# Performance work log

Hardware: AMD Instinct MI355X
Metric: run time of the kernel (lower is better)

## Reference

```python
import jax, jax.numpy as jnp
import numpy as np

B, T, C = 128, 256, 384
H, D = 6, 64

def setup_inputs() -> dict:
    key = jax.random.key(0)
    ks = jax.random.split(key, 6)
    s = 1.0 / np.sqrt(C)
    return {
        "x": jax.random.normal(ks[0], (B, T, C), dtype=jnp.float32),
        "Wq": jax.random.normal(ks[1], (H, C, D), dtype=jnp.float32) * s,
        "Wk": jax.random.normal(ks[2], (H, C, D), dtype=jnp.float32) * s,
        "Wv": jax.random.normal(ks[3], (H, C, D), dtype=jnp.float32) * s,
        "Wp": jax.random.normal(ks[4], (C, C), dtype=jnp.float32) * s,
        "bp": jnp.zeros((C,), dtype=jnp.float32),
    }

def reference(x, Wq, Wk, Wv, Wp, bp):
    # per-head projections (all heads at once): [B,T,C] x [H,C,D] -> [B,H,T,D]
    q = jnp.einsum("btc,hcd->bhtd", x, Wq)
    k = jnp.einsum("btc,hcd->bhtd", x, Wk)
    v = jnp.einsum("btc,hcd->bhtd", x, Wv)
    scale = 1.0 / jnp.sqrt(jnp.asarray(D, dtype=x.dtype))
    # scores [B,H,T,T], causal mask, softmax
    wei = jnp.einsum("bhqd,bhkd->bhqk", q, k) * scale
    causal = jnp.tril(jnp.ones((T, T), dtype=bool))
    wei = jnp.where(causal, wei, -jnp.inf)
    wei = jax.nn.softmax(wei, axis=-1)
    # dropout layers are identity in eval mode
    out = jnp.einsum("bhqk,bhkd->bhqd", wei, v)
    # concat heads: [B,T,H*D]
    out = out.transpose(0, 2, 1, 3).reshape(B, T, H * D)
    return out @ Wp + bp
```

## Files before the change

### kernel.cpp

```cpp
#include <hip/hip_runtime.h>
#include <stdint.h>


typedef __attribute__((ext_vector_type(8))) short bf16x8;
typedef __attribute__((ext_vector_type(4))) float f32x4;
typedef __attribute__((ext_vector_type(16))) float f32x16;

__device__ __forceinline__ unsigned short f2b(float f) {
    union { float f; unsigned int u; } v; v.f = f;
    unsigned int u = v.u + 0x7fffu + ((v.u >> 16) & 1u);
    return (unsigned short)(u >> 16);
}

__device__ __forceinline__ unsigned int pk2(float lo, float hi) {
    return (unsigned int)f2b(lo) | ((unsigned int)f2b(hi) << 16);
}

__device__ __forceinline__ uint32_t cvtpk(float lo, float hi) {
    uint32_t r;
    asm("v_cvt_pk_bf16_f32 %0, %1, %2" : "=v"(r) : "v"(lo), "v"(hi));
    return r;
}

__device__ __forceinline__ void gload_lds16(const void* g, void* lds) {
    auto gp = reinterpret_cast<const __attribute__((address_space(1))) uint32_t*>(
        reinterpret_cast<uintptr_t>(g));
    auto lp = reinterpret_cast<__attribute__((address_space(3))) uint32_t*>(
        reinterpret_cast<uintptr_t>(lds));
    __builtin_amdgcn_global_load_lds(gp, lp, 16, 0, 0);
}

#define SBAR0() __builtin_amdgcn_sched_barrier(0)


__global__ void cvt_w_kernel(const float* __restrict__ Wq, const float* __restrict__ Wk,
                             const float* __restrict__ Wv, const float* __restrict__ Wp,
                             unsigned short* __restrict__ wt, unsigned short* __restrict__ wpt) {
    int i = blockIdx.x * 256 + threadIdx.x;
    if (i >= 589824) return;
    if (i < 442368) {
        int j = i / 384, c = i - j * 384;
        int p = j / 384, rem = j - p * 384;
        int h = rem >> 6, d = rem & 63;
        const float* W = (p == 0) ? Wq : ((p == 1) ? Wk : Wv);
        wt[i] = f2b(W[(size_t)(h * 384 + c) * 64 + d]);
    } else {
        int i2 = i - 442368;
        int n = i2 / 384, c = i2 - n * 384;
        wpt[i2] = f2b(Wp[(size_t)c * 384 + n]);
    }
}


__global__ __launch_bounds__(256, 4) void gemm_qkv(
    const float* __restrict__ x,
    const unsigned short* __restrict__ wt,
    unsigned short* __restrict__ qO,
    unsigned short* __restrict__ kO,
    unsigned short* __restrict__ vO)
{
    extern __shared__ __align__(16) unsigned short smem[];
    unsigned short* As0 = smem;
    unsigned short* As1 = smem + 4096;
    unsigned short* Bs0 = smem + 8192;
    unsigned short* Bs1 = smem + 12288;

    const int tid  = threadIdx.x;
    const int lane = tid & 63;
    const int w    = tid >> 6;
    const int wm = w >> 1, wn = w & 1;

    const int flat = blockIdx.y * 9 + blockIdx.x;
    const int swz = (flat & 7) * 288 + (flat >> 3);
    const int bx = swz % 9, by = swz / 9;
    const int col0 = bx * 128;
    const int row0 = by * 128;

    f32x4 acc[4][4];
#pragma unroll
    for (int mf = 0; mf < 4; ++mf)
#pragma unroll
        for (int nf = 0; nf < 4; ++nf)
#pragma unroll
            for (int r = 0; r < 4; ++r) acc[mf][nf][r] = 0.f;

    const int ci0 = tid;
    const int ci1 = tid + 256;
    const float* aS0 = x + (size_t)(row0 + (ci0 >> 2)) * 384 + (ci0 & 3) * 8;
    const float* aS1 = x + (size_t)(row0 + (ci1 >> 2)) * 384 + (ci1 & 3) * 8;
    const unsigned short* bS0 = wt + (size_t)(col0 + (ci0 >> 2)) * 384 + (ci0 & 3) * 8;
    const unsigned short* bS1 = wt + (size_t)(col0 + (ci1 >> 2)) * 384 + (ci1 & 3) * 8;
    const int cb = w * 64;

    float4 aReg0, aReg1, aReg2, aReg3;
    auto LOADA = [&](int kt) {
        const float* p0 = aS0 + kt * 32;
        const float* p1 = aS1 + kt * 32;
        aReg0 = *(const float4*)(p0);
        aReg1 = *(const float4*)(p0 + 4);
        aReg2 = *(const float4*)(p1);
        aReg3 = *(const float4*)(p1 + 4);
    };
    auto WRITEA = [&](unsigned short* As) {
        uint4 w0, w1;
        w0.x = cvtpk(aReg0.x, aReg0.y); w0.y = cvtpk(aReg0.z, aReg0.w);
        w0.z = cvtpk(aReg1.x, aReg1.y); w0.w = cvtpk(aReg1.z, aReg1.w);
        w1.x = cvtpk(aReg2.x, aReg2.y); w1.y = cvtpk(aReg2.z, aReg2.w);
        w1.z = cvtpk(aReg3.x, aReg3.y); w1.w = cvtpk(aReg3.z, aReg3.w);
        *(uint4*)&As[ci0 * 8] = w0;
        *(uint4*)&As[ci1 * 8] = w1;
    };
    auto STAGEB = [&](unsigned short* Bs, int kt) {
        gload_lds16(bS0 + kt * 32, Bs + (cb + 0) * 8);
        gload_lds16(bS1 + kt * 32, Bs + (cb + 256) * 8);
    };
    auto COMPUTE = [&](const unsigned short* A, const unsigned short* B) {
        bf16x8 aF[4], bF[4];
#pragma unroll
        for (int mf = 0; mf < 4; ++mf)
            aF[mf] = *(const bf16x8*)&A[(wm * 64 + mf * 16 + (lane & 15)) * 32 + (lane >> 4) * 8];
#pragma unroll
        for (int nf = 0; nf < 4; ++nf)
            bF[nf] = *(const bf16x8*)&B[(wn * 64 + nf * 16 + (lane & 15)) * 32 + (lane >> 4) * 8];
#pragma unroll
        for (int mf = 0; mf < 4; ++mf)
#pragma unroll
            for (int nf = 0; nf < 4; ++nf)
                acc[mf][nf] = __builtin_amdgcn_mfma_f32_16x16x32_bf16(aF[mf], bF[nf], acc[mf][nf], 0, 0, 0);
    };

    LOADA(0);
    STAGEB(Bs0, 0);
    WRITEA(As0);
    __syncthreads();

    for (int t = 0; t < 12; ++t) {
        unsigned short* Acur = (t & 1) ? As1 : As0;
        unsigned short* Bcur = (t & 1) ? Bs1 : Bs0;
        unsigned short* Anx  = (t & 1) ? As0 : As1;
        unsigned short* Bnx  = (t & 1) ? Bs0 : Bs1;
        if (t < 11) {
            LOADA(t + 1);
            STAGEB(Bnx, t + 1);
        }
        COMPUTE(Acur, Bcur);
        if (t < 11) WRITEA(Anx);
        __syncthreads();
    }

    unsigned short* Ct = smem;
    const int co = tid & 15;
    const int rr = tid >> 4;
    const int colg = col0 + co * 8;
    const int p = colg / 384;
    const int rem = colg - p * 384;
    const int h = rem >> 6;
    const int d = rem & 63;
    unsigned short* dst = (p == 0) ? qO : ((p == 1) ? kO : vO);

#pragma unroll
    for (int ph = 0; ph < 2; ++ph) {
        if (wm == ph) {
#pragma unroll
            for (int mf = 0; mf < 4; ++mf)
#pragma unroll
                for (int nf = 0; nf < 4; ++nf)
#pragma unroll
                    for (int r = 0; r < 4; ++r)
                        Ct[(mf * 16 + (lane >> 4) * 4 + r) * 136 + wn * 64 + nf * 16 + (lane & 15)] =
                            f2b(acc[mf][nf][r]);
        }
        __syncthreads();
#pragma unroll
        for (int it = 0; it < 4; ++it) {
            const int r_loc = it * 16 + rr;
            const int m = row0 + ph * 64 + r_loc;
            const int b = m >> 8, t = m & 255;
            uint4 val = *(const uint4*)&Ct[r_loc * 136 + co * 8];
            *(uint4*)&dst[(size_t)((b * 6 + h) * 256 + t) * 64 + d] = val;
        }
        __syncthreads();
    }
}


__global__ __launch_bounds__(512, 4) void attn_kernel(
    const unsigned short* __restrict__ Qg,
    const unsigned short* __restrict__ Kg,
    const unsigned short* __restrict__ Vg,
    unsigned short* __restrict__ Og)
{
    extern __shared__ __align__(16) unsigned short asmem[];
    unsigned short* Ks = asmem;
    unsigned short* Vs = asmem + 256 * 72;
    unsigned short* Ot = asmem;
    const int bh = blockIdx.x;
    const int b = bh / 6, h = bh - b * 6;
    const int tid = threadIdx.x;
    const int lane = tid & 63;
    const int w = tid >> 6;
    const int lo = lane & 31, hi = lane >> 5;

    const unsigned short* kg = Kg + (size_t)bh * 256 * 64;
#pragma unroll
    for (int j = 0; j < 4; ++j) {
        int chunk = tid + 512 * j;
        int key = chunk >> 3, dc = (chunk & 7) * 8;
        *(uint4*)&Ks[key * 72 + dc] = *(const uint4*)&kg[key * 64 + dc];
    }
    {
        const unsigned short* vg = Vg + (size_t)bh * 256 * 64;
        uint32_t* Vs32 = (uint32_t*)Vs;
#pragma unroll
        for (int i = 0; i < 2; ++i) {
            int u = tid + 512 * i;
            int t2 = (u & 31) | ((u >> 8) << 5);
            int dm = (u >> 5) & 7;
            uint4 r0 = *(const uint4*)&vg[(2 * t2 + 0) * 64 + dm * 8];
            uint4 r1 = *(const uint4*)&vg[(2 * t2 + 1) * 64 + dm * 8];
            const unsigned short* e0 = (const unsigned short*)&r0;
            const unsigned short* e1 = (const unsigned short*)&r1;
#pragma unroll
            for (int j = 0; j < 8; ++j)
                Vs32[(dm * 8 + j) * 132 + t2] = (uint32_t)e0[j] | ((uint32_t)e1[j] << 16);
        }
    }
    __syncthreads();

    const int q0 = w * 32;
    const unsigned short* qg = Qg + (size_t)bh * 256 * 64 + (size_t)(q0 + lo) * 64 + hi * 8;
    bf16x8 qF[4];
#pragma unroll
    for (int dc = 0; dc < 4; ++dc) qF[dc] = *(const bf16x8*)(qg + dc * 16);

    float m = -1e30f, ssum = 0.f;
    f32x16 o0, o1;
#pragma unroll
    for (int r = 0; r < 16; ++r) { o0[r] = 0.f; o1[r] = 0.f; }

    for (int kt = 0; kt <= w; ++kt) {
        f32x16 s;
#pragma unroll
        for (int r = 0; r < 16; ++r) s[r] = 0.f;
        __builtin_amdgcn_s_setprio(1);
#pragma unroll
        for (int dc = 0; dc < 4; ++dc) {
            bf16x8 aK = *(const bf16x8*)&Ks[(kt * 32 + lo) * 72 + dc * 16 + hi * 8];
            s = __builtin_amdgcn_mfma_f32_32x32x16_bf16(aK, qF[dc], s, 0, 0, 0);
        }
        __builtin_amdgcn_s_setprio(0);
        float p[16];
        float pmax = -1e30f;
        const bool diag = (kt == w);
#pragma unroll
        for (int r = 0; r < 16; ++r) {
            float sv = s[r] * 0.125f;
            const int keyl = (r & 3) + 8 * (r >> 2) + 4 * hi;
            if (diag && keyl > lo) sv = -1e30f;
            p[r] = sv;
            pmax = fmaxf(pmax, sv);
        }
        pmax = fmaxf(pmax, __shfl_xor(pmax, 32, 64));
        if (pmax > m + 8.f) {
            const float sf = __expf(m - pmax);
            m = pmax;
            ssum *= sf;
#pragma unroll
            for (int r = 0; r < 16; ++r) { o0[r] *= sf; o1[r] *= sf; }
        }
        float rs = 0.f;
#pragma unroll
        for (int r = 0; r < 16; ++r) { p[r] = __expf(p[r] - m); rs += p[r]; }
        rs += __shfl_xor(rs, 32, 64);
        ssum += rs;

        union { unsigned short u[16]; bf16x8 v[2]; } P;
        {
            float recv[4];
#pragma unroll
            for (int j2 = 0; j2 < 4; ++j2) {
                float sendv = hi ? p[j2] : p[4 + j2];
                recv[j2] = __shfl_xor(sendv, 32, 64);
            }
#pragma unroll
            for (int i = 0; i < 4; ++i) P.u[i]     = f2b(hi ? recv[i] : p[i]);
#pragma unroll
            for (int i = 0; i < 4; ++i) P.u[4 + i] = f2b(hi ? p[4 + i] : recv[i]);
        }
        {
            float recv[4];
#pragma unroll
            for (int j2 = 0; j2 < 4; ++j2) {
                float sendv = hi ? p[8 + j2] : p[12 + j2];
                recv[j2] = __shfl_xor(sendv, 32, 64);
            }
#pragma unroll
            for (int i = 0; i < 4; ++i) P.u[8 + i]  = f2b(hi ? recv[i] : p[8 + i]);
#pragma unroll
            for (int i = 0; i < 4; ++i) P.u[12 + i] = f2b(hi ? p[12 + i] : recv[i]);
        }

        __builtin_amdgcn_s_setprio(1);
#pragma unroll
        for (int kc = 0; kc < 2; ++kc) {
            bf16x8 aV0 = *(const bf16x8*)&Vs[lo * 264 + kt * 32 + kc * 16 + hi * 8];
            o0 = __builtin_amdgcn_mfma_f32_32x32x16_bf16(aV0, P.v[kc], o0, 0, 0, 0);
            bf16x8 aV1 = *(const bf16x8*)&Vs[(32 + lo) * 264 + kt * 32 + kc * 16 + hi * 8];
            o1 = __builtin_amdgcn_mfma_f32_32x32x16_bf16(aV1, P.v[kc], o1, 0, 0, 0);
        }
        __builtin_amdgcn_s_setprio(0);
    }

    __syncthreads();
    const float inv = 1.f / ssum;
    {
        uint32_t* ot32 = (uint32_t*)&Ot[w * 32 * 72];
#pragma unroll
        for (int g = 0; g < 4; ++g) {
            const int dbase0 = 8 * g + 4 * hi;
            uint32_t w0 = pk2(o0[4 * g + 0] * inv, o0[4 * g + 1] * inv);
            uint32_t w1 = pk2(o0[4 * g + 2] * inv, o0[4 * g + 3] * inv);
            int dw = lo * 36 + (dbase0 >> 1);
            ot32[dw] = w0;
            ot32[dw + 1] = w1;
            uint32_t w2 = pk2(o1[4 * g + 0] * inv, o1[4 * g + 1] * inv);
            uint32_t w3 = pk2(o1[4 * g + 2] * inv, o1[4 * g + 3] * inv);
            int dw1 = lo * 36 + ((32 + dbase0) >> 1);
            ot32[dw1] = w2;
            ot32[dw1 + 1] = w3;
        }
    }
    __syncthreads();
    {
        const unsigned short* ot = &Ot[w * 32 * 72];
        const int q = lane >> 1;
        const int half = (lane & 1) * 32;
        unsigned short* og = Og + (size_t)(b * 256 + q0 + q) * 384 + h * 64 + half;
#pragma unroll
        for (int jj = 0; jj < 4; ++jj) {
            uint4 val = *(const uint4*)&ot[q * 72 + half + jj * 8];
            *(uint4*)&og[jj * 8] = val;
        }
    }
}


__global__ __launch_bounds__(256, 3) void gemm_proj(
    const unsigned short* __restrict__ ob,
    const unsigned short* __restrict__ wpt,
    const float* __restrict__ bp,
    float* __restrict__ out)
{
    __shared__ __align__(16) unsigned short As[3][128 * 32];
    __shared__ __align__(16) unsigned short Bs[3][128 * 32];
    const int tid  = threadIdx.x;
    const int lane = tid & 63;
    const int w    = tid >> 6;
    const int wm = w >> 1, wn = w & 1;

    const int flat = blockIdx.y * 3 + blockIdx.x;
    const int swz = (flat & 7) * 96 + (flat >> 3);
    const int bx = swz % 3, by = swz / 3;
    const int col0 = bx * 128;
    const int row0 = by * 128;

    const unsigned short* Abase = ob  + (size_t)row0 * 384;
    const unsigned short* Bbase = wpt + (size_t)col0 * 384;

    f32x4 acc[4][4];
#pragma unroll
    for (int mf = 0; mf < 4; ++mf)
#pragma unroll
        for (int nf = 0; nf < 4; ++nf)
#pragma unroll
            for (int r = 0; r < 4; ++r) acc[mf][nf][r] = 0.f;

    const int ci0 = tid;
    const int ci1 = tid + 256;
    const int r0c = ci0 >> 2, o0c = (ci0 & 3) ^ ((ci0 >> 3) & 3);
    const int r1c = ci1 >> 2, o1c = (ci1 & 3) ^ ((ci1 >> 3) & 3);
    const unsigned short* aSrc0 = Abase + (size_t)r0c * 384 + o0c * 8;
    const unsigned short* aSrc1 = Abase + (size_t)r1c * 384 + o1c * 8;
    const unsigned short* bSrc0 = Bbase + (size_t)r0c * 384 + o0c * 8;
    const unsigned short* bSrc1 = Bbase + (size_t)r1c * 384 + o1c * 8;
    const int cb = w * 64;

    auto STAGE = [&](int buf, int kt) {
        const int k0_ = kt * 32;
        gload_lds16(aSrc0 + k0_, (unsigned short*)As[buf] + (cb + 0) * 8);
        gload_lds16(bSrc0 + k0_, (unsigned short*)Bs[buf] + (cb + 0) * 8);
        gload_lds16(aSrc1 + k0_, (unsigned short*)As[buf] + (cb + 256) * 8);
        gload_lds16(bSrc1 + k0_, (unsigned short*)Bs[buf] + (cb + 256) * 8);
    };

    const int fr = lane & 15;
    const int oc = (lane >> 4) ^ ((fr >> 1) & 3);

    auto COMPUTE = [&](int buf) {
        const unsigned short* A = As[buf];
        const unsigned short* B = Bs[buf];
        bf16x8 aF[4], bF[4];
#pragma unroll
        for (int mf = 0; mf < 4; ++mf)
            aF[mf] = *(const bf16x8*)&A[(wm * 64 + mf * 16 + fr) * 32 + oc * 8];
#pragma unroll
        for (int nf = 0; nf < 4; ++nf)
            bF[nf] = *(const bf16x8*)&B[(wn * 64 + nf * 16 + fr) * 32 + oc * 8];
#pragma unroll
        for (int mf = 0; mf < 4; ++mf)
#pragma unroll
            for (int nf = 0; nf < 4; ++nf)
                acc[mf][nf] = __builtin_amdgcn_mfma_f32_16x16x32_bf16(aF[mf], bF[nf], acc[mf][nf], 0, 0, 0);
    };

    STAGE(0, 0);
    STAGE(1, 1);
    SBAR0();
    int bufS = 2, bufC = 0;
    for (int t = 0; t < 10; ++t) {
        STAGE(bufS, t + 2);
        bufS = (bufS == 2) ? 0 : bufS + 1;
        SBAR0();
        asm volatile("s_waitcnt vmcnt(8)" ::: "memory");
        SBAR0();
        __builtin_amdgcn_s_barrier();
        SBAR0();
        COMPUTE(bufC);
        bufC = (bufC == 2) ? 0 : bufC + 1;
        SBAR0();
        __builtin_amdgcn_s_barrier();
        SBAR0();
    }
    asm volatile("s_waitcnt vmcnt(4)" ::: "memory");
    SBAR0();
    __builtin_amdgcn_s_barrier();
    SBAR0();
    COMPUTE(1);
    SBAR0();
    __builtin_amdgcn_s_barrier();
    SBAR0();
    asm volatile("s_waitcnt vmcnt(0)" ::: "memory");
    SBAR0();
    __builtin_amdgcn_s_barrier();
    SBAR0();
    COMPUTE(2);

#pragma unroll
    for (int nf = 0; nf < 4; ++nf) {
        const int col = col0 + wn * 64 + nf * 16 + (lane & 15);
        const float bias = bp[col];
#pragma unroll
        for (int mf = 0; mf < 4; ++mf) {
            const int mbase = row0 + wm * 64 + mf * 16 + ((lane >> 4) * 4);
#pragma unroll
            for (int r = 0; r < 4; ++r) {
                const int mrow = mbase + r;
                out[(size_t)mrow * 384 + col] = acc[mf][nf][r] + bias;
            }
        }
    }
}


extern "C" void kernel_launch(void* const* d_in, const int* in_sizes, int n_in,
                              void* d_out, int out_size, void* d_ws, size_t ws_size,
                              hipStream_t stream) {
    const float* x  = (const float*)d_in[0];
    const float* Wq = (const float*)d_in[1];
    const float* Wk = (const float*)d_in[2];
    const float* Wv = (const float*)d_in[3];
    const float* Wp = (const float*)d_in[4];
    const float* bp = (const float*)d_in[5];
    float* out = (float*)d_out;

    char* ws = (char*)d_ws;
    unsigned short* ob  = (unsigned short*)(ws);
    unsigned short* qb  = (unsigned short*)(ws + 25165824);
    unsigned short* kb  = (unsigned short*)(ws + 50331648);
    unsigned short* vb  = (unsigned short*)(ws + 75497472);
    unsigned short* wt  = (unsigned short*)(ws + 100663296);
    unsigned short* wpt = (unsigned short*)(ws + 101548032);

    cvt_w_kernel<<<2304, 256, 0, stream>>>(Wq, Wk, Wv, Wp, wt, wpt);
    gemm_qkv<<<dim3(9, 256), 256, 32768, stream>>>(x, wt, qb, kb, vb);
    attn_kernel<<<768, 512, 70656, stream>>>(qb, kb, vb, ob);
    gemm_proj<<<dim3(3, 256), 256, 0, stream>>>(ob, wpt, bp, out);
}
```

Before: 105.2 us.

## Fuse QKV projection into attention kernel per batch-head block

Each attention block now computes its own head's Q, K and V projections from x via MFMA and writes them straight into LDS, eliminating the separate QKV GEMM kernel and its global Q/K/V writes and reads. It also swizzles the LDS staging layout to reduce bank conflicts. In exchange x is re-read once per head, the block uses about 128 KB of LDS limiting occupancy to one block per CU, and the GEMM tile per block is small and serialized before attention.

```diff
diff --git a/kernel.cpp b/kernel.cpp
--- a/kernel.cpp
+++ b/kernel.cpp
@@ -52,45 +52,58 @@
 }
 
 
-__global__ __launch_bounds__(256, 4) void gemm_qkv(
+__global__ __launch_bounds__(512, 1) void qkv_attn(
     const float* __restrict__ x,
-    const unsigned short* __restrict__ wt,
-    unsigned short* __restrict__ qO,
-    unsigned short* __restrict__ kO,
-    unsigned short* __restrict__ vO)
+    const unsigned short* __restrict__ wtb,
+    unsigned short* __restrict__ Og)
 {
-    extern __shared__ __align__(16) unsigned short smem[];
-    unsigned short* As0 = smem;
-    unsigned short* As1 = smem + 4096;
-    unsigned short* Bs0 = smem + 8192;
-    unsigned short* Bs1 = smem + 12288;
-
-    const int tid  = threadIdx.x;
+    extern __shared__ __align__(16) unsigned short fsm[];
+    unsigned short* Ks  = fsm;
+    unsigned short* Vs  = fsm + 18432;
+    unsigned short* Stg = fsm + 35328;
+    unsigned short* As0 = Stg;
+    unsigned short* As1 = Stg + 8192;
+    unsigned short* Bs0 = Stg + 16384;
+    unsigned short* Bs1 = Stg + 22528;
+    unsigned short* Qs  = Stg;
+    unsigned short* Ot  = Stg;
+
+    const int bh = blockIdx.x;
+    const int b = bh / 6, h = bh - b * 6;
+    const int tid = threadIdx.x;
     const int lane = tid & 63;
-    const int w    = tid >> 6;
+    const int w = tid >> 6;
     const int wm = w >> 1, wn = w & 1;
-
-    const int flat = blockIdx.y * 9 + blockIdx.x;
-    const int swz = (flat & 7) * 288 + (flat >> 3);
-    const int bx = swz % 9, by = swz / 9;
-    const int col0 = bx * 128;
-    const int row0 = by * 128;
-
-    f32x4 acc[4][4];
+    const int fr = lane & 15, q4 = lane >> 4;
+    const int lo = lane & 31, hi = lane >> 5;
+
+    const float* xrow = x + (size_t)b * 256 * 384;
+
+    const int aci0 = tid, aci1 = tid + 512;
+    const int ar0 = aci0 >> 2, aog0 = aci0 & 3;
+    const int ar1 = aci1 >> 2, aog1 = aci1 & 3;
+    const float* aS0 = xrow + (size_t)ar0 * 384 + aog0 * 8;
+    const float* aS1 = xrow + (size_t)ar1 * 384 + aog1 * 8;
+    const int ad0 = ar0 * 32 + (aog0 ^ ((ar0 >> 1) & 3)) * 8;
+    const int ad1 = ar1 * 32 + (aog1 ^ ((ar1 >> 1) & 3)) * 8;
+
+    const int bci0 = tid;
+    const int bp0 = bci0 >> 8, brs0 = (bci0 >> 2) & 63;
+    const int bog0 = (bci0 & 3) ^ ((bci0 >> 3) & 3);
+    const unsigned short* bS0 = wtb + (size_t)(bp0 * 384 + h * 64 + brs0) * 384 + bog0 * 8;
+    const int bci1 = 512 + tid;
+    const int bp1 = bci1 >> 8, brs1 = (bci1 >> 2) & 63;
+    const int bog1 = (bci1 & 3) ^ ((bci1 >> 3) & 3);
+    const unsigned short* bS1 = wtb + (size_t)(bp1 * 384 + h * 64 + brs1) * 384 + bog1 * 8;
+    const int cbB = w * 64;
+
+    f32x4 acc[4][6];
 #pragma unroll
     for (int mf = 0; mf < 4; ++mf)
 #pragma unroll
-        for (int nf = 0; nf < 4; ++nf)
+        for (int nf = 0; nf < 6; ++nf)
 #pragma unroll
             for (int r = 0; r < 4; ++r) acc[mf][nf][r] = 0.f;
-
-    const int ci0 = tid;
-    const int ci1 = tid + 256;
-    const float* aS0 = x + (size_t)(row0 + (ci0 >> 2)) * 384 + (ci0 & 3) * 8;
-    const float* aS1 = x + (size_t)(row0 + (ci1 >> 2)) * 384 + (ci1 & 3) * 8;
-    const unsigned short* bS0 = wt + (size_t)(col0 + (ci0 >> 2)) * 384 + (ci0 & 3) * 8;
-    const unsigned short* bS1 = wt + (size_t)(col0 + (ci1 >> 2)) * 384 + (ci1 & 3) * 8;
-    const int cb = w * 64;
 
     float4 aReg0, aReg1, aReg2, aReg3;
     auto LOADA = [&](int kt) {
@@ -107,25 +120,26 @@
         w0.z = cvtpk(aReg1.x, aReg1.y); w0.w = cvtpk(aReg1.z, aReg1.w);
         w1.x = cvtpk(aReg2.x, aReg2.y); w1.y = cvtpk(aReg2.z, aReg2.w);
         w1.z = cvtpk(aReg3.x, aReg3.y); w1.w = cvtpk(aReg3.z, aReg3.w);
-        *(uint4*)&As[ci0 * 8] = w0;
-        *(uint4*)&As[ci1 * 8] = w1;
+        *(uint4*)&As[ad0] = w0;
+        *(uint4*)&As[ad1] = w1;
     };
     auto STAGEB = [&](unsigned short* Bs, int kt) {
-        gload_lds16(bS0 + kt * 32, Bs + (cb + 0) * 8);
-        gload_lds16(bS1 + kt * 32, Bs + (cb + 256) * 8);
-    };
+        gload_lds16(bS0 + kt * 32, Bs + cbB * 8);
+        if (tid < 256) gload_lds16(bS1 + kt * 32, Bs + (512 + cbB) * 8);
+    };
+    const int ocf = q4 ^ ((fr >> 1) & 3);
     auto COMPUTE = [&](const unsigned short* A, const unsigned short* B) {
-        bf16x8 aF[4], bF[4];
+        bf16x8 aF[4], bF[6];
 #pragma unroll
         for (int mf = 0; mf < 4; ++mf)
-            aF[mf] = *(const bf16x8*)&A[(wm * 64 + mf * 16 + (lane & 15)) * 32 + (lane >> 4) * 8];
-#pragma unroll
-        for (int nf = 0; nf < 4; ++nf)
-            bF[nf] = *(const bf16x8*)&B[(wn * 64 + nf * 16 + (lane & 15)) * 32 + (lane >> 4) * 8];
+            aF[mf] = *(const bf16x8*)&A[(wm * 64 + mf * 16 + fr) * 32 + ocf * 8];
+#pragma unroll
+        for (int nf = 0; nf < 6; ++nf)
+            bF[nf] = *(const bf16x8*)&B[(wn * 96 + nf * 16 + fr) * 32 + ocf * 8];
 #pragma unroll
         for (int mf = 0; mf < 4; ++mf)
 #pragma unroll
-            for (int nf = 0; nf < 4; ++nf)
+            for (int nf = 0; nf < 6; ++nf)
                 acc[mf][nf] = __builtin_amdgcn_mfma_f32_16x16x32_bf16(aF[mf], bF[nf], acc[mf][nf], 0, 0, 0);
     };
 
@@ -148,90 +162,31 @@
         __syncthreads();
     }
 
-    unsigned short* Ct = smem;
-    const int co = tid & 15;
-    const int rr = tid >> 4;
-    const int colg = col0 + co * 8;
-    const int p = colg / 384;
-    const int rem = colg - p * 384;
-    const int h = rem >> 6;
-    const int d = rem & 63;
-    unsigned short* dst = (p == 0) ? qO : ((p == 1) ? kO : vO);
-
-#pragma unroll
-    for (int ph = 0; ph < 2; ++ph) {
-        if (wm == ph) {
-#pragma unroll
-            for (int mf = 0; mf < 4; ++mf)
-#pragma unroll
-                for (int nf = 0; nf < 4; ++nf)
-#pragma unroll
-                    for (int r = 0; r < 4; ++r)
-                        Ct[(mf * 16 + (lane >> 4) * 4 + r) * 136 + wn * 64 + nf * 16 + (lane & 15)] =
-                            f2b(acc[mf][nf][r]);
-        }
-        __syncthreads();
-#pragma unroll
-        for (int it = 0; it < 4; ++it) {
-            const int r_loc = it * 16 + rr;
-            const int m = row0 + ph * 64 + r_loc;
-            const int b = m >> 8, t = m & 255;
-            uint4 val = *(const uint4*)&Ct[r_loc * 136 + co * 8];
-            *(uint4*)&dst[(size_t)((b * 6 + h) * 256 + t) * 64 + d] = val;
-        }
-        __syncthreads();
-    }
-}
-
-
-__global__ __launch_bounds__(512, 4) void attn_kernel(
-    const unsigned short* __restrict__ Qg,
-    const unsigned short* __restrict__ Kg,
-    const unsigned short* __restrict__ Vg,
-    unsigned short* __restrict__ Og)
-{
-    extern __shared__ __align__(16) unsigned short asmem[];
-    unsigned short* Ks = asmem;
-    unsigned short* Vs = asmem + 256 * 72;
-    unsigned short* Ot = asmem;
-    const int bh = blockIdx.x;
-    const int b = bh / 6, h = bh - b * 6;
-    const int tid = threadIdx.x;
-    const int lane = tid & 63;
-    const int w = tid >> 6;
-    const int lo = lane & 31, hi = lane >> 5;
-
-    const unsigned short* kg = Kg + (size_t)bh * 256 * 64;
-#pragma unroll
-    for (int j = 0; j < 4; ++j) {
-        int chunk = tid + 512 * j;
-        int key = chunk >> 3, dc = (chunk & 7) * 8;
-        *(uint4*)&Ks[key * 72 + dc] = *(const uint4*)&kg[key * 64 + dc];
-    }
-    {
-        const unsigned short* vg = Vg + (size_t)bh * 256 * 64;
-        uint32_t* Vs32 = (uint32_t*)Vs;
-#pragma unroll
-        for (int i = 0; i < 2; ++i) {
-            int u = tid + 512 * i;
-            int t2 = (u & 31) | ((u >> 8) << 5);
-            int dm = (u >> 5) & 7;
-            uint4 r0 = *(const uint4*)&vg[(2 * t2 + 0) * 64 + dm * 8];
-            uint4 r1 = *(const uint4*)&vg[(2 * t2 + 1) * 64 + dm * 8];
-            const unsigned short* e0 = (const unsigned short*)&r0;
-            const unsigned short* e1 = (const unsigned short*)&r1;
-#pragma unroll
-            for (int j = 0; j < 8; ++j)
-                Vs32[(dm * 8 + j) * 132 + t2] = (uint32_t)e0[j] | ((uint32_t)e1[j] << 16);
+#pragma unroll
+    for (int nf = 0; nf < 6; ++nf) {
+        const int jbase = wn * 96 + nf * 16;
+        const int tgt = jbase >> 6;
+        const int d = (jbase & 63) + fr;
+#pragma unroll
+        for (int mf = 0; mf < 4; ++mf) {
+            const int tb = wm * 64 + mf * 16 + q4 * 4;
+#pragma unroll
+            for (int r = 0; r < 4; ++r) {
+                const unsigned short val = f2b(acc[mf][nf][r]);
+                const int t = tb + r;
+                if (tgt == 0)      Qs[t * 72 + d] = val;
+                else if (tgt == 1) Ks[t * 72 + d] = val;
+                else               Vs[d * 264 + t] = val;
+            }
         }
     }
     __syncthreads();
 
     const int q0 = w * 32;
-    const unsigned short* qg = Qg + (size_t)bh * 256 * 64 + (size_t)(q0 + lo) * 64 + hi * 8;
     bf16x8 qF[4];
 #pragma unroll
-    for (int dc = 0; dc < 4; ++dc) qF[dc] = *(const bf16x8*)(qg + dc * 16);
+    for (int dc = 0; dc < 4; ++dc)
+        qF[dc] = *(const bf16x8*)&Qs[(q0 + lo) * 72 + dc * 16 + hi * 8];
 
     float m = -1e30f, ssum = 0.f;
     f32x16 o0, o1;
@@ -475,14 +430,10 @@
 
     char* ws = (char*)d_ws;
     unsigned short* ob  = (unsigned short*)(ws);
-    unsigned short* qb  = (unsigned short*)(ws + 25165824);
-    unsigned short* kb  = (unsigned short*)(ws + 50331648);
-    unsigned short* vb  = (unsigned short*)(ws + 75497472);
-    unsigned short* wt  = (unsigned short*)(ws + 100663296);
-    unsigned short* wpt = (unsigned short*)(ws + 101548032);
+    unsigned short* wt  = (unsigned short*)(ws + 25165824);
+    unsigned short* wpt = (unsigned short*)(ws + 26050560);
 
     cvt_w_kernel<<<2304, 256, 0, stream>>>(Wq, Wk, Wv, Wp, wt, wpt);
-    gemm_qkv<<<dim3(9, 256), 256, 32768, stream>>>(x, wt, qb, kb, vb);
-    attn_kernel<<<768, 512, 70656, stream>>>(qb, kb, vb, ob);
+    qkv_attn<<<768, 512, 128000, stream>>>(x, wt, ob);
     gemm_proj<<<dim3(3, 256), 256, 0, stream>>>(ob, wpt, bp, out);
 }
```

Result: slower. 119.6 us (+13.7%).

## Double K-tile depth in QKV GEMM and XOR-swizzle LDS layout

Applied to the files above, without the earlier changes.

The QKV projection GEMM now stages a 64-wide K slice per iteration instead of 32, which halves the number of main-loop iterations and barriers. The LDS tiles for A and B use an XOR swizzle on 16-byte chunks to avoid bank conflicts when the MFMA fragments are read. Shared memory per block doubles to 64KB and launch bounds drop from 4 to 2 blocks per CU, so occupancy falls in exchange for fewer syncs and conflict-free LDS reads.

```diff
diff --git a/kernel.cpp b/kernel.cpp
--- a/kernel.cpp
+++ b/kernel.cpp
@@ -52,7 +52,7 @@
 }
 
 
-__global__ __launch_bounds__(256, 4) void gemm_qkv(
+__global__ __launch_bounds__(256, 2) void gemm_qkv(
     const float* __restrict__ x,
     const unsigned short* __restrict__ wt,
     unsigned short* __restrict__ qO,
@@ -61,9 +61,9 @@
 {
     extern __shared__ __align__(16) unsigned short smem[];
     unsigned short* As0 = smem;
-    unsigned short* As1 = smem + 4096;
-    unsigned short* Bs0 = smem + 8192;
-    unsigned short* Bs1 = smem + 12288;
+    unsigned short* As1 = smem + 8192;
+    unsigned short* Bs0 = smem + 16384;
+    unsigned short* Bs1 = smem + 24576;
 
     const int tid  = threadIdx.x;
     const int lane = tid & 63;
@@ -84,49 +84,74 @@
 #pragma unroll
             for (int r = 0; r < 4; ++r) acc[mf][nf][r] = 0.f;
 
-    const int ci0 = tid;
-    const int ci1 = tid + 256;
-    const float* aS0 = x + (size_t)(row0 + (ci0 >> 2)) * 384 + (ci0 & 3) * 8;
-    const float* aS1 = x + (size_t)(row0 + (ci1 >> 2)) * 384 + (ci1 & 3) * 8;
-    const unsigned short* bS0 = wt + (size_t)(col0 + (ci0 >> 2)) * 384 + (ci0 & 3) * 8;
-    const unsigned short* bS1 = wt + (size_t)(col0 + (ci1 >> 2)) * 384 + (ci1 & 3) * 8;
-    const int cb = w * 64;
-
-    float4 aReg0, aReg1, aReg2, aReg3;
+    const float* aS[4];
+    int aD[4];
+    const unsigned short* bS[4];
+#pragma unroll
+    for (int j = 0; j < 4; ++j) {
+        const int ci = tid + 256 * j;
+        const int row = ci >> 3, og = ci & 7;
+        aS[j] = x + (size_t)(row0 + row) * 384 + og * 8;
+        aD[j] = row * 64 + (og ^ (row & 7)) * 8;
+        bS[j] = wt + (size_t)(col0 + row) * 384 + (og ^ (row & 7)) * 8;
+    }
+    const int cbB = w * 64;
+
+    float4 aR0, aR1, aR2, aR3, aR4, aR5, aR6, aR7;
     auto LOADA = [&](int kt) {
-        const float* p0 = aS0 + kt * 32;
-        const float* p1 = aS1 + kt * 32;
-        aReg0 = *(const float4*)(p0);
-        aReg1 = *(const float4*)(p0 + 4);
-        aReg2 = *(const float4*)(p1);
-        aReg3 = *(const float4*)(p1 + 4);
+        const int k0_ = kt * 64;
+        aR0 = *(const float4*)(aS[0] + k0_); aR1 = *(const float4*)(aS[0] + k0_ + 4);
+        aR2 = *(const float4*)(aS[1] + k0_); aR3 = *(const float4*)(aS[1] + k0_ + 4);
+        aR4 = *(const float4*)(aS[2] + k0_); aR5 = *(const float4*)(aS[2] + k0_ + 4);
+        aR6 = *(const float4*)(aS[3] + k0_); aR7 = *(const float4*)(aS[3] + k0_ + 4);
     };
     auto WRITEA = [&](unsigned short* As) {
-        uint4 w0, w1;
-        w0.x = cvtpk(aReg0.x, aReg0.y); w0.y = cvtpk(aReg0.z, aReg0.w);
-        w0.z = cvtpk(aReg1.x, aReg1.y); w0.w = cvtpk(aReg1.z, aReg1.w);
-        w1.x = cvtpk(aReg2.x, aReg2.y); w1.y = cvtpk(aReg2.z, aReg2.w);
-        w1.z = cvtpk(aReg3.x, aReg3.y); w1.w = cvtpk(aReg3.z, aReg3.w);
-        *(uint4*)&As[ci0 * 8] = w0;
-        *(uint4*)&As[ci1 * 8] = w1;
+        uint4 w0, w1, w2, w3;
+        w0.x = cvtpk(aR0.x, aR0.y); w0.y = cvtpk(aR0.z, aR0.w);
+        w0.z = cvtpk(aR1.x, aR1.y); w0.w = cvtpk(aR1.z, aR1.w);
+        w1.x = cvtpk(aR2.x, aR2.y); w1.y = cvtpk(aR2.z, aR2.w);
+        w1.z = cvtpk(aR3.x, aR3.y); w1.w = cvtpk(aR3.z, aR3.w);
+        w2.x = cvtpk(aR4.x, aR4.y); w2.y = cvtpk(aR4.z, aR4.w);
+        w2.z = cvtpk(aR5.x, aR5.y); w2.w = cvtpk(aR5.z, aR5.w);
+        w3.x = cvtpk(aR6.x, aR6.y); w3.y = cvtpk(aR6.z, aR6.w);
+        w3.z = cvtpk(aR7.x, aR7.y); w3.w = cvtpk(aR7.z, aR7.w);
+        *(uint4*)&As[aD[0]] = w0;
+        *(uint4*)&As[aD[1]] = w1;
+        *(uint4*)&As[aD[2]] = w2;
+        *(uint4*)&As[aD[3]] = w3;
     };
     auto STAGEB = [&](unsigned short* Bs, int kt) {
-        gload_lds16(bS0 + kt * 32, Bs + (cb + 0) * 8);
-        gload_lds16(bS1 + kt * 32, Bs + (cb + 256) * 8);
+        const int k0_ = kt * 64;
+        gload_lds16(bS[0] + k0_, Bs + (cbB + 0) * 8);
+        gload_lds16(bS[1] + k0_, Bs + (cbB + 256) * 8);
+        gload_lds16(bS[2] + k0_, Bs + (cbB + 512) * 8);
+        gload_lds16(bS[3] + k0_, Bs + (cbB + 768) * 8);
     };
+
+    const int fr = lane & 15;
+    const int q4 = lane >> 4;
+
     auto COMPUTE = [&](const unsigned short* A, const unsigned short* B) {
-        bf16x8 aF[4], bF[4];
-#pragma unroll
-        for (int mf = 0; mf < 4; ++mf)
-            aF[mf] = *(const bf16x8*)&A[(wm * 64 + mf * 16 + (lane & 15)) * 32 + (lane >> 4) * 8];
-#pragma unroll
-        for (int nf = 0; nf < 4; ++nf)
-            bF[nf] = *(const bf16x8*)&B[(wn * 64 + nf * 16 + (lane & 15)) * 32 + (lane >> 4) * 8];
-#pragma unroll
-        for (int mf = 0; mf < 4; ++mf)
-#pragma unroll
-            for (int nf = 0; nf < 4; ++nf)
-                acc[mf][nf] = __builtin_amdgcn_mfma_f32_16x16x32_bf16(aF[mf], bF[nf], acc[mf][nf], 0, 0, 0);
+#pragma unroll
+        for (int kk = 0; kk < 2; ++kk) {
+            const int ocx = (kk * 4 + q4);
+            bf16x8 aF[4], bF[4];
+#pragma unroll
+            for (int mf = 0; mf < 4; ++mf) {
+                const int row = wm * 64 + mf * 16 + fr;
+                aF[mf] = *(const bf16x8*)&A[row * 64 + (ocx ^ (fr & 7)) * 8];
+            }
+#pragma unroll
+            for (int nf = 0; nf < 4; ++nf) {
+                const int row = wn * 64 + nf * 16 + fr;
+                bF[nf] = *(const bf16x8*)&B[row * 64 + (ocx ^ (fr & 7)) * 8];
+            }
+#pragma unroll
+            for (int mf = 0; mf < 4; ++mf)
+#pragma unroll
+                for (int nf = 0; nf < 4; ++nf)
+                    acc[mf][nf] = __builtin_amdgcn_mfma_f32_16x16x32_bf16(aF[mf], bF[nf], acc[mf][nf], 0, 0, 0);
+        }
     };
 
     LOADA(0);
@@ -134,17 +159,17 @@
     WRITEA(As0);
     __syncthreads();
 
-    for (int t = 0; t < 12; ++t) {
+    for (int t = 0; t < 6; ++t) {
         unsigned short* Acur = (t & 1) ? As1 : As0;
         unsigned short* Bcur = (t & 1) ? Bs1 : Bs0;
         unsigned short* Anx  = (t & 1) ? As0 : As1;
         unsigned short* Bnx  = (t & 1) ? Bs0 : Bs1;
-        if (t < 11) {
+        if (t < 5) {
             LOADA(t + 1);
             STAGEB(Bnx, t + 1);
         }
         COMPUTE(Acur, Bcur);
-        if (t < 11) WRITEA(Anx);
+        if (t < 5) WRITEA(Anx);
         __syncthreads();
     }
 
@@ -482,7 +507,7 @@
     unsigned short* wpt = (unsigned short*)(ws + 101548032);
 
     cvt_w_kernel<<<2304, 256, 0, stream>>>(Wq, Wk, Wv, Wp, wt, wpt);
-    gemm_qkv<<<dim3(9, 256), 256, 32768, stream>>>(x, wt, qb, kb, vb);
+    gemm_qkv<<<dim3(9, 256), 256, 65536, stream>>>(x, wt, qb, kb, vb);
     attn_kernel<<<768, 512, 70656, stream>>>(qb, kb, vb, ob);
     gemm_proj<<<dim3(3, 256), 256, 0, stream>>>(ob, wpt, bp, out);
 }
```

New measurement: 109.5 us. +4.1%, slower.
